# Kernel optimization log

Measured on AMD Instinct MI355X. Metric: run time of the kernel, lower is better.

Reference implementation:

```python
import jax, jax.numpy as jnp
import numpy as np

N_GRAPHS = 256
STEPS = 3


def setup_inputs() -> dict:
    key = jax.random.key(0)
    ks = jax.random.split(key, 8)
    N, d, out = 100000, 512, 256
    s = 0.05
    x = jax.random.normal(ks[0], (N, d), dtype=jnp.float32)
    batch = jnp.sort(jax.random.randint(ks[1], (N,), 0, N_GRAPHS)).astype(jnp.int64)
    W_ih = jax.random.normal(ks[2], (4 * d, 2 * d), dtype=jnp.float32) * s
    W_hh = jax.random.normal(ks[3], (4 * d, d), dtype=jnp.float32) * s
    b_ih = jax.random.normal(ks[4], (4 * d,), dtype=jnp.float32) * s
    b_hh = jax.random.normal(ks[5], (4 * d,), dtype=jnp.float32) * s
    W_proj = jax.random.normal(ks[6], (out, 2 * d), dtype=jnp.float32) * s
    b_proj = jax.random.normal(ks[7], (out,), dtype=jnp.float32) * s
    return {"x": x, "batch": batch, "W_ih": W_ih, "W_hh": W_hh,
            "b_ih": b_ih, "b_hh": b_hh, "W_proj": W_proj, "b_proj": b_proj}


def _set2set(x, batch, W_ih, W_hh, b_ih, b_hh):
    N, d = x.shape
    B = N_GRAPHS
    h = jnp.zeros((B, d), x.dtype)
    c = jnp.zeros((B, d), x.dtype)
    q_star = jnp.zeros((B, 2 * d), x.dtype)
    for _ in range(STEPS):
        # single-step LSTM cell (PyTorch gate order i,f,g,o)
        gates = q_star @ W_ih.T + b_ih + h @ W_hh.T + b_hh
        i, f, g, o = jnp.split(gates, 4, axis=-1)
        c = jax.nn.sigmoid(f) * c + jax.nn.sigmoid(i) * jnp.tanh(g)
        h = jax.nn.sigmoid(o) * jnp.tanh(c)
        q = h                                   # [B, d]
        # segment softmax attention over nodes
        e = jnp.sum(x * q[batch], axis=-1)      # [N]
        m = jax.ops.segment_max(e, batch, num_segments=B)
        m = jnp.where(jnp.isfinite(m), m, 0.0)  # guard empty segments
        ex = jnp.exp(e - m[batch])
        denom = jax.ops.segment_sum(ex, batch, num_segments=B) + 1e-16
        a = ex / denom[batch]                   # [N]
        r = jax.ops.segment_sum(a[:, None] * x, batch, num_segments=B)  # [B, d]
        q_star = jnp.concatenate([q, r], axis=-1)
    return q_star


def reference(x, batch, W_ih, W_hh, b_ih, b_hh, W_proj, b_proj):
    pooled = _set2set(x, batch, W_ih, W_hh, b_ih, b_hh)  # [B, 2d]
    return pooled @ W_proj.T + b_proj                    # [B, out]
```

## Files before the change

kernel.cpp:

```cpp
#include <hip/hip_runtime.h>
#include <hip/hip_bf16.h>


typedef __bf16 bf16_t;
typedef __bf16 bf16x8 __attribute__((ext_vector_type(8)));
typedef float  f32x4  __attribute__((ext_vector_type(4)));

#define D     512
#define B_GR  256
#define FOURD 2048
#define KCAT  1536
#define AWAVES 16
#define DET_BLOCKS 400

__device__ __forceinline__ float load_f(const void* b, int i, int f32) {
    return f32 ? ((const float*)b)[i] : (float)((const bf16_t*)b)[i];
}

__global__ void detect_part1(const int* __restrict__ b32, int N,
                             const unsigned short* __restrict__ xh,
                             int* __restrict__ partA, int* __restrict__ partB) {
    __shared__ int sA, sB;
    if (threadIdx.x == 0) { sA = 0; sB = 0; }
    __syncthreads();
    int gid = blockIdx.x * blockDim.x + threadIdx.x;
    int stride = gridDim.x * blockDim.x;
    int dec = 0;
    for (int i = gid; i < N - 1; i += stride)
        if (b32[i] > b32[i + 1]) dec = 1;
    int bad = 0;
    for (int i = gid; i < 1024; i += stride) {
        unsigned e = (xh[i] >> 7) & 0xff;
        if (e >= 134) bad = 1;
    }
    if (dec) atomicOr(&sA, 1);
    if (bad) atomicOr(&sB, 1);
    __syncthreads();
    if (threadIdx.x == 0) { partA[blockIdx.x] = sA; partB[blockIdx.x] = sB; }
}

__global__ void detect_part2(const int* __restrict__ partA,
                             const int* __restrict__ partB, int nblk,
                             int* __restrict__ flags) {
    __shared__ int sA, sB;
    if (threadIdx.x == 0) { sA = 0; sB = 0; }
    __syncthreads();
    int a = 0, b = 0;
    for (int i = threadIdx.x; i < nblk; i += blockDim.x) {
        a |= partA[i];
        b |= partB[i];
    }
    if (a) atomicOr(&sA, 1);
    if (b) atomicOr(&sB, 1);
    __syncthreads();
    if (threadIdx.x == 0) { flags[0] = sA; flags[1] = sB; }
}

#define WCAT_E (FOURD * KCAT)
#define WP_E   (256 * 1024)
__global__ void prep_seg_kernel(const void* __restrict__ W_ih,
                                const void* __restrict__ W_hh,
                                const void* __restrict__ b_ih,
                                const void* __restrict__ b_hh,
                                const void* __restrict__ W_proj,
                                const void* __restrict__ b_proj,
                                const void* __restrict__ batch, int N, int B,
                                const int* __restrict__ flags,
                                bf16_t* __restrict__ Wcat, bf16_t* __restrict__ Wp,
                                float* __restrict__ bsum, float* __restrict__ bp,
                                int* __restrict__ seg) {
    const int f32 = flags[1];
    int gid = blockIdx.x * blockDim.x + threadIdx.x;
    int stride = gridDim.x * blockDim.x;

    if (gid < N) {
        const int n = gid;
        const int is64 = flags[0];
        const int* b32 = (const int*)batch;
        const long long* b64 = (const long long*)batch;
        int cur = is64 ? (int)b64[n] : b32[n];
        if (n == 0) {
            for (int b = 0; b <= cur && b <= B; ++b) seg[b] = 0;
        } else {
            int prev = is64 ? (int)b64[n - 1] : b32[n - 1];
            for (int b = prev + 1; b <= cur && b <= B; ++b) seg[b] = n;
        }
        if (n == N - 1) {
            for (int b = cur + 1; b <= B; ++b) seg[b] = N;
        }
    }

    const int total = WCAT_E + WP_E + FOURD + 256;
    for (int idx = gid; idx < total; idx += stride) {
        if (idx < WCAT_E) {
            int r = idx / KCAT, k = idx - r * KCAT;
            float v = (k < 1024) ? load_f(W_ih, r * 1024 + k, f32)
                                 : load_f(W_hh, r * 512 + (k - 1024), f32);
            Wcat[idx] = (bf16_t)v;
        } else if (idx < WCAT_E + WP_E) {
            int j = idx - WCAT_E;
            Wp[j] = (bf16_t)load_f(W_proj, j, f32);
        } else if (idx < WCAT_E + WP_E + FOURD) {
            int i = idx - WCAT_E - WP_E;
            bsum[i] = load_f(b_ih, i, f32) + load_f(b_hh, i, f32);
        } else {
            int i = idx - WCAT_E - WP_E - FOURD;
            bp[i] = load_f(b_proj, i, f32);
        }
    }
}

__device__ __forceinline__ void lstm0_math(const float* __restrict__ bsum,
                                           int t, float& cn, float& hn) {
    float gi = bsum[t], gg = bsum[1024 + t], go = bsum[1536 + t];
    float si = 1.f / (1.f + __expf(-gi));
    float so = 1.f / (1.f + __expf(-go));
    float tg = tanhf(gg);
    cn = si * tg;
    hn = so * tanhf(cn);
}

__global__ __launch_bounds__(64)
void gemm_lstm(const bf16_t* __restrict__ AbufIn,
               const bf16_t* __restrict__ Wcat,
               const float* __restrict__ bsum,
               float* __restrict__ c, float* __restrict__ h,
               bf16_t* __restrict__ AbufOut) {
    const int lane  = threadIdx.x;
    const int t0    = blockIdx.x * 16;
    const int m0    = blockIdx.y * 16;
    const int rowA  = m0 + (lane & 15);
    const int colB  = t0 + (lane & 15);
    const int kbase = (lane >> 4) * 8;

    f32x4 acc[4] = {{0,0,0,0},{0,0,0,0},{0,0,0,0},{0,0,0,0}};

    for (int k0 = 0; k0 < KCAT; k0 += 32) {
        int k = k0 + kbase;
        bf16x8 a = *(const bf16x8*)(AbufIn + (size_t)rowA * KCAT + k);
#pragma unroll
        for (int g = 0; g < 4; ++g) {
            bf16x8 bfr = *(const bf16x8*)(Wcat + (size_t)(g * 512 + colB) * KCAT + k);
            acc[g] = __builtin_amdgcn_mfma_f32_16x16x32_bf16(a, bfr, acc[g], 0, 0, 0);
        }
    }

    const int col   = colB;
    const int rbase = (lane >> 4) * 4;
    float bi = bsum[col], bf = bsum[512 + col], bg = bsum[1024 + col], bo = bsum[1536 + col];
#pragma unroll
    for (int r = 0; r < 4; ++r) {
        int m = m0 + rbase + r;
        float gi = acc[0][r] + bi;
        float gf = acc[1][r] + bf;
        float gg = acc[2][r] + bg;
        float go = acc[3][r] + bo;
        size_t ci = (size_t)m * D + col;
        float cv = c[ci];
        float si = 1.f / (1.f + __expf(-gi));
        float sf = 1.f / (1.f + __expf(-gf));
        float so = 1.f / (1.f + __expf(-go));
        float tg = tanhf(gg);
        float cn = sf * cv + si * tg;
        float hn = so * tanhf(cn);
        c[ci] = cn;
        h[ci] = hn;
        bf16_t hb = (bf16_t)hn;
        AbufOut[(size_t)m * KCAT + col]        = hb;
        AbufOut[(size_t)m * KCAT + 1024 + col] = hb;
    }
}


template<bool WRXB>
__device__ __forceinline__ void scan_f32(const float* __restrict__ xp,
                                         bf16_t* __restrict__ xb,
                                         int s, int cnt, int wave, int lane,
                                         const float* hl,
                                         float& m_w, float& s_w, float* r_w) {
    int i = 4 * wave;
    for (; i + 4 <= cnt; i += 4 * AWAVES) {
        size_t off = (((size_t)(s + i)) << 9) + (size_t)(lane * 8);
        float xr[4][8];
#pragma unroll
        for (int r = 0; r < 4; ++r) {
            const float* p = xp + off + (size_t)r * D;
            float4 v0 = *(const float4*)p;
            float4 v1 = *(const float4*)(p + 4);
            xr[r][0] = v0.x; xr[r][1] = v0.y; xr[r][2] = v0.z; xr[r][3] = v0.w;
            xr[r][4] = v1.x; xr[r][5] = v1.y; xr[r][6] = v1.z; xr[r][7] = v1.w;
        }
        if (WRXB) {
#pragma unroll
            for (int r = 0; r < 4; ++r) {
                bf16x8 v;
#pragma unroll
                for (int j = 0; j < 8; ++j) v[j] = (bf16_t)xr[r][j];
                *(bf16x8*)(xb + off + (size_t)r * D) = v;
            }
        }
        float d[4] = {0.f, 0.f, 0.f, 0.f};
#pragma unroll
        for (int j = 0; j < 8; ++j) {
#pragma unroll
            for (int r = 0; r < 4; ++r) d[r] += xr[r][j] * hl[j];
        }
#pragma unroll
        for (int o = 32; o > 0; o >>= 1) {
#pragma unroll
            for (int r = 0; r < 4; ++r) d[r] += __shfl_xor(d[r], o, 64);
        }
        float mx    = fmaxf(fmaxf(d[0], d[1]), fmaxf(d[2], d[3]));
        float m_new = fmaxf(m_w, mx);
        float alpha = __expf(m_w - m_new);
        float p0 = __expf(d[0] - m_new), p1 = __expf(d[1] - m_new);
        float p2 = __expf(d[2] - m_new), p3 = __expf(d[3] - m_new);
        s_w = s_w * alpha + ((p0 + p1) + (p2 + p3));
#pragma unroll
        for (int j = 0; j < 8; ++j)
            r_w[j] = r_w[j] * alpha + p0 * xr[0][j] + p1 * xr[1][j]
                                    + p2 * xr[2][j] + p3 * xr[3][j];
        m_w = m_new;
    }
    if (i < cnt) {
        int rem = cnt - i;
        size_t off = (((size_t)(s + i)) << 9) + (size_t)(lane * 8);
        float xr[4][8];
#pragma unroll
        for (int r = 0; r < 4; ++r) {
            if (r < rem) {
                const float* p = xp + off + (size_t)r * D;
                float4 v0 = *(const float4*)p;
                float4 v1 = *(const float4*)(p + 4);
                xr[r][0] = v0.x; xr[r][1] = v0.y; xr[r][2] = v0.z; xr[r][3] = v0.w;
                xr[r][4] = v1.x; xr[r][5] = v1.y; xr[r][6] = v1.z; xr[r][7] = v1.w;
            } else {
#pragma unroll
                for (int j = 0; j < 8; ++j) xr[r][j] = 0.f;
            }
        }
        if (WRXB) {
#pragma unroll
            for (int r = 0; r < 4; ++r) {
                if (r < rem) {
                    bf16x8 v;
#pragma unroll
                    for (int j = 0; j < 8; ++j) v[j] = (bf16_t)xr[r][j];
                    *(bf16x8*)(xb + off + (size_t)r * D) = v;
                }
            }
        }
        float d[4] = {0.f, 0.f, 0.f, 0.f};
#pragma unroll
        for (int j = 0; j < 8; ++j) {
#pragma unroll
            for (int r = 0; r < 4; ++r) d[r] += xr[r][j] * hl[j];
        }
#pragma unroll
        for (int o = 32; o > 0; o >>= 1) {
#pragma unroll
            for (int r = 0; r < 4; ++r) d[r] += __shfl_xor(d[r], o, 64);
        }
#pragma unroll
        for (int r = 0; r < 4; ++r)
            if (r >= rem) d[r] = -INFINITY;
        float mx    = fmaxf(fmaxf(d[0], d[1]), fmaxf(d[2], d[3]));
        float m_new = fmaxf(m_w, mx);
        float alpha = __expf(m_w - m_new);
        float p0 = __expf(d[0] - m_new), p1 = __expf(d[1] - m_new);
        float p2 = __expf(d[2] - m_new), p3 = __expf(d[3] - m_new);
        s_w = s_w * alpha + ((p0 + p1) + (p2 + p3));
#pragma unroll
        for (int j = 0; j < 8; ++j)
            r_w[j] = r_w[j] * alpha + p0 * xr[0][j] + p1 * xr[1][j]
                                    + p2 * xr[2][j] + p3 * xr[3][j];
        m_w = m_new;
    }
}

__device__ __forceinline__ void scan_bf16(const bf16_t* __restrict__ xp,
                                          int s, int cnt, int wave, int lane,
                                          const float* hl,
                                          float& m_w, float& s_w, float* r_w) {
    int i = 4 * wave;
    for (; i + 4 <= cnt; i += 4 * AWAVES) {
        size_t off = (((size_t)(s + i)) << 9) + (size_t)(lane * 8);
        float xr[4][8];
#pragma unroll
        for (int r = 0; r < 4; ++r) {
            bf16x8 v = *(const bf16x8*)(xp + off + (size_t)r * D);
#pragma unroll
            for (int j = 0; j < 8; ++j) xr[r][j] = (float)v[j];
        }
        float d[4] = {0.f, 0.f, 0.f, 0.f};
#pragma unroll
        for (int j = 0; j < 8; ++j) {
#pragma unroll
            for (int r = 0; r < 4; ++r) d[r] += xr[r][j] * hl[j];
        }
#pragma unroll
        for (int o = 32; o > 0; o >>= 1) {
#pragma unroll
            for (int r = 0; r < 4; ++r) d[r] += __shfl_xor(d[r], o, 64);
        }
        float mx    = fmaxf(fmaxf(d[0], d[1]), fmaxf(d[2], d[3]));
        float m_new = fmaxf(m_w, mx);
        float alpha = __expf(m_w - m_new);
        float p0 = __expf(d[0] - m_new), p1 = __expf(d[1] - m_new);
        float p2 = __expf(d[2] - m_new), p3 = __expf(d[3] - m_new);
        s_w = s_w * alpha + ((p0 + p1) + (p2 + p3));
#pragma unroll
        for (int j = 0; j < 8; ++j)
            r_w[j] = r_w[j] * alpha + p0 * xr[0][j] + p1 * xr[1][j]
                                    + p2 * xr[2][j] + p3 * xr[3][j];
        m_w = m_new;
    }
    if (i < cnt) {
        int rem = cnt - i;
        size_t off = (((size_t)(s + i)) << 9) + (size_t)(lane * 8);
        float xr[4][8];
#pragma unroll
        for (int r = 0; r < 4; ++r) {
            if (r < rem) {
                bf16x8 v = *(const bf16x8*)(xp + off + (size_t)r * D);
#pragma unroll
                for (int j = 0; j < 8; ++j) xr[r][j] = (float)v[j];
            } else {
#pragma unroll
                for (int j = 0; j < 8; ++j) xr[r][j] = 0.f;
            }
        }
        float d[4] = {0.f, 0.f, 0.f, 0.f};
#pragma unroll
        for (int j = 0; j < 8; ++j) {
#pragma unroll
            for (int r = 0; r < 4; ++r) d[r] += xr[r][j] * hl[j];
        }
#pragma unroll
        for (int o = 32; o > 0; o >>= 1) {
#pragma unroll
            for (int r = 0; r < 4; ++r) d[r] += __shfl_xor(d[r], o, 64);
        }
#pragma unroll
        for (int r = 0; r < 4; ++r)
            if (r >= rem) d[r] = -INFINITY;
        float mx    = fmaxf(fmaxf(d[0], d[1]), fmaxf(d[2], d[3]));
        float m_new = fmaxf(m_w, mx);
        float alpha = __expf(m_w - m_new);
        float p0 = __expf(d[0] - m_new), p1 = __expf(d[1] - m_new);
        float p2 = __expf(d[2] - m_new), p3 = __expf(d[3] - m_new);
        s_w = s_w * alpha + ((p0 + p1) + (p2 + p3));
#pragma unroll
        for (int j = 0; j < 8; ++j)
            r_w[j] = r_w[j] * alpha + p0 * xr[0][j] + p1 * xr[1][j]
                                    + p2 * xr[2][j] + p3 * xr[3][j];
        m_w = m_new;
    }
}

template<int STEP0, int USE_XB, int PROJ>
__global__ __launch_bounds__(1024)
void attention_kernel(const void* __restrict__ x, bf16_t* __restrict__ xb,
                      int N, const int* __restrict__ seg,
                      const float* __restrict__ hbuf,
                      const float* __restrict__ bsum,
                      float* __restrict__ c_buf,
                      bf16_t* __restrict__ AbufOut,
                      const bf16_t* __restrict__ Wp,
                      const float* __restrict__ bp,
                      void* __restrict__ out,
                      const int* __restrict__ flags) {
    __shared__ float racc2[AWAVES][D];
    __shared__ float red_m[AWAVES], red_s[AWAVES];
    __shared__ __align__(16) bf16_t qsb[PROJ ? 1024 : 1];
    __shared__ float pout[PROJ ? 4 : 1][PROJ ? 256 : 1];

    const int f32x = flags[1];

    const int b = blockIdx.x;
    int s  = seg[b];
    int en = seg[b + 1];
    s  = (s  < 0) ? 0 : ((s  > N) ? N : s);
    en = (en < s) ? s : ((en > N) ? N : en);
    const int cnt  = en - s;
    const int tid  = threadIdx.x;
    const int wave = tid >> 6;
    const int lane = tid & 63;

    float hl[8];
    if (STEP0) {
#pragma unroll
        for (int j = 0; j < 8; ++j) {
            float cn, hn;
            lstm0_math(bsum, lane * 8 + j, cn, hn);
            hl[j] = hn;
        }
    } else {
        const float* hp = hbuf + ((size_t)b << 9) + lane * 8;
#pragma unroll
        for (int j = 0; j < 8; ++j) hl[j] = hp[j];
    }

    float m_w = -INFINITY, s_w = 0.f;
    float r_w[8];
#pragma unroll
    for (int j = 0; j < 8; ++j) r_w[j] = 0.f;

    if (f32x) {
        if (STEP0 || !USE_XB) {
            scan_f32<(STEP0 && USE_XB)>((const float*)x, xb, s, cnt,
                                        wave, lane, hl, m_w, s_w, r_w);
        } else {
            scan_bf16(xb, s, cnt, wave, lane, hl, m_w, s_w, r_w);
        }
    } else {
        scan_bf16((const bf16_t*)x, s, cnt, wave, lane, hl, m_w, s_w, r_w);
    }

    if (lane == 0) { red_m[wave] = m_w; red_s[wave] = s_w; }
    __syncthreads();

    float M = -INFINITY, S = 0.f;
#pragma unroll
    for (int w = 0; w < AWAVES; ++w)
        if (red_s[w] > 0.f) M = fmaxf(M, red_m[w]);
#pragma unroll
    for (int w = 0; w < AWAVES; ++w)
        if (red_s[w] > 0.f) S += red_s[w] * __expf(red_m[w] - M);
    float Sinv  = 1.f / (S + 1e-16f);
    float scale = (s_w > 0.f) ? __expf(m_w - M) * Sinv : 0.f;

#pragma unroll
    for (int j = 0; j < 8; ++j) racc2[wave][lane * 8 + j] = r_w[j] * scale;
    __syncthreads();

    if (PROJ) {
        if (tid < D) {
            float r = 0.f;
#pragma unroll
            for (int w = 0; w < AWAVES; ++w) r += racc2[w][tid];
            qsb[512 + tid] = (bf16_t)r;
            qsb[tid] = (bf16_t)hbuf[((size_t)b << 9) + tid];
        }
        __syncthreads();
        const int o    = tid & 255;
        const int part = tid >> 8;
        float acc = 0.f;
#pragma unroll
        for (int kk = 0; kk < 256; kk += 8) {
            int k = part * 256 + kk;
            bf16x8 w = *(const bf16x8*)(Wp + (size_t)o * 1024 + k);
            bf16x8 q = *(const bf16x8*)(qsb + k);
#pragma unroll
            for (int j = 0; j < 8; ++j) acc += (float)q[j] * (float)w[j];
        }
        pout[part][o] = acc;
        __syncthreads();
        if (tid < 256) {
            float v = pout[0][tid] + pout[1][tid] + pout[2][tid] + pout[3][tid]
                    + bp[tid];
            if (f32x) ((float*)out)[(size_t)b * 256 + tid]  = v;
            else      ((bf16_t*)out)[(size_t)b * 256 + tid] = (bf16_t)v;
        }
    } else {
        if (tid < D) {
            float r = 0.f;
#pragma unroll
            for (int w = 0; w < AWAVES; ++w) r += racc2[w][tid];
            AbufOut[(size_t)b * KCAT + 512 + tid] = (bf16_t)r;
            if (STEP0) {
                float cn, hn;
                lstm0_math(bsum, tid, cn, hn);
                c_buf[((size_t)b << 9) + tid] = cn;
                bf16_t hb = (bf16_t)hn;
                AbufOut[(size_t)b * KCAT + tid]        = hb;
                AbufOut[(size_t)b * KCAT + 1024 + tid] = hb;
            }
        }
    }
}

extern "C" void kernel_launch(void* const* d_in, const int* in_sizes, int n_in,
                              void* d_out, int out_size, void* d_ws, size_t ws_size,
                              hipStream_t stream) {
    const void* x      = d_in[0];
    const void* batch  = d_in[1];
    const void* W_ih   = d_in[2];
    const void* W_hh   = d_in[3];
    const void* b_ih   = d_in[4];
    const void* b_hh   = d_in[5];
    const void* W_proj = d_in[6];
    const void* b_proj = d_in[7];

    const int N = in_sizes[1];
    const int B = B_GR;

    char* p = (char*)d_ws;
    size_t used = 0;
    auto carve = [&](size_t bytes) {
        void* r = (void*)p;
        size_t a = (bytes + 1023) & ~(size_t)1023;
        p += a;
        used += a;
        return r;
    };
    float*  c_buf = (float*)carve((size_t)B * D * 4);
    float*  h_buf = (float*)carve((size_t)B * D * 4);
    bf16_t* Abuf0 = (bf16_t*)carve((size_t)B * KCAT * 2);
    bf16_t* Abuf1 = (bf16_t*)carve((size_t)B * KCAT * 2);
    bf16_t* Wcat  = (bf16_t*)carve((size_t)FOURD * KCAT * 2);
    bf16_t* Wp    = (bf16_t*)carve((size_t)256 * 1024 * 2);
    float*  bsum  = (float*)carve((size_t)FOURD * 4);
    float*  bp    = (float*)carve((size_t)256 * 4);
    int*    seg   = (int*)carve((size_t)(B + 1) * 4);
    int*    flags = (int*)carve(8);
    int*    partA = (int*)carve(DET_BLOCKS * 4);
    int*    partB = (int*)carve(DET_BLOCKS * 4);
    if (used > ws_size) return;
    bf16_t* xb = (bf16_t*)carve((size_t)N * D * 2);
    int use_xb = (used <= ws_size) ? 1 : 0;

    detect_part1<<<DET_BLOCKS, 256, 0, stream>>>(
        (const int*)batch, N, (const unsigned short*)x, partA, partB);
    detect_part2<<<1, 512, 0, stream>>>(partA, partB, DET_BLOCKS, flags);
    prep_seg_kernel<<<1024, 256, 0, stream>>>(W_ih, W_hh, b_ih, b_hh,
                                              W_proj, b_proj, batch, N, B,
                                              flags, Wcat, Wp, bsum, bp, seg);

    if (use_xb)
        attention_kernel<1, 1, 0><<<B, 1024, 0, stream>>>(
            x, xb, N, seg, h_buf, bsum, c_buf, Abuf0, Wp, bp, d_out, flags);
    else
        attention_kernel<1, 0, 0><<<B, 1024, 0, stream>>>(
            x, xb, N, seg, h_buf, bsum, c_buf, Abuf0, Wp, bp, d_out, flags);

    gemm_lstm<<<dim3(D / 16, B / 16), 64, 0, stream>>>(
        Abuf0, Wcat, bsum, c_buf, h_buf, Abuf1);
    if (use_xb)
        attention_kernel<0, 1, 0><<<B, 1024, 0, stream>>>(
            x, xb, N, seg, h_buf, bsum, c_buf, Abuf1, Wp, bp, d_out, flags);
    else
        attention_kernel<0, 0, 0><<<B, 1024, 0, stream>>>(
            x, xb, N, seg, h_buf, bsum, c_buf, Abuf1, Wp, bp, d_out, flags);

    gemm_lstm<<<dim3(D / 16, B / 16), 64, 0, stream>>>(
        Abuf1, Wcat, bsum, c_buf, h_buf, Abuf0);
    if (use_xb)
        attention_kernel<0, 1, 1><<<B, 1024, 0, stream>>>(
            x, xb, N, seg, h_buf, bsum, c_buf, Abuf0, Wp, bp, d_out, flags);
    else
        attention_kernel<0, 0, 1><<<B, 1024, 0, stream>>>(
            x, xb, N, seg, h_buf, bsum, c_buf, Abuf0, Wp, bp, d_out, flags);
}
```

Baseline: 443.0 us.

## Fuse attention and LSTM GEMM steps into one cooperative persistent kernel

Replaces the five separate attention and GEMM launches with a single cooperative kernel of 256 blocks that uses grid-wide barriers between phases, with two waves per block running the GEMM tiles. Segment-bound computation is split out of the weight-prep kernel into its own launch. The aim is to remove launch gaps and kernel-boundary drains between the dependent steps. In exchange, each GEMM phase runs on only two waves per block while the rest idle, grid.sync adds its own cost, and the whole grid must be co-resident.

```diff
diff --git a/kernel.cpp b/kernel.cpp
--- a/kernel.cpp
+++ b/kernel.cpp
@@ -1,5 +1,8 @@
 #include <hip/hip_runtime.h>
 #include <hip/hip_bf16.h>
+#include <hip/hip_cooperative_groups.h>
+
+namespace cg = cooperative_groups;
 
 
 typedef __bf16 bf16_t;
@@ -56,40 +59,40 @@
     if (threadIdx.x == 0) { flags[0] = sA; flags[1] = sB; }
 }
 
+__global__ void seg_bounds_kernel(const void* __restrict__ batch, int N, int B,
+                                  const int* __restrict__ flags,
+                                  int* __restrict__ seg) {
+    int n = blockIdx.x * blockDim.x + threadIdx.x;
+    if (n >= N) return;
+    const int is64 = flags[0];
+    const int* b32 = (const int*)batch;
+    const long long* b64 = (const long long*)batch;
+    int cur = is64 ? (int)b64[n] : b32[n];
+    if (n == 0) {
+        for (int b = 0; b <= cur && b <= B; ++b) seg[b] = 0;
+    } else {
+        int prev = is64 ? (int)b64[n - 1] : b32[n - 1];
+        for (int b = prev + 1; b <= cur && b <= B; ++b) seg[b] = n;
+    }
+    if (n == N - 1) {
+        for (int b = cur + 1; b <= B; ++b) seg[b] = N;
+    }
+}
+
 #define WCAT_E (FOURD * KCAT)
 #define WP_E   (256 * 1024)
-__global__ void prep_seg_kernel(const void* __restrict__ W_ih,
-                                const void* __restrict__ W_hh,
-                                const void* __restrict__ b_ih,
-                                const void* __restrict__ b_hh,
-                                const void* __restrict__ W_proj,
-                                const void* __restrict__ b_proj,
-                                const void* __restrict__ batch, int N, int B,
-                                const int* __restrict__ flags,
-                                bf16_t* __restrict__ Wcat, bf16_t* __restrict__ Wp,
-                                float* __restrict__ bsum, float* __restrict__ bp,
-                                int* __restrict__ seg) {
+__global__ void prep_kernel(const void* __restrict__ W_ih,
+                            const void* __restrict__ W_hh,
+                            const void* __restrict__ b_ih,
+                            const void* __restrict__ b_hh,
+                            const void* __restrict__ W_proj,
+                            const void* __restrict__ b_proj,
+                            const int* __restrict__ flags,
+                            bf16_t* __restrict__ Wcat, bf16_t* __restrict__ Wp,
+                            float* __restrict__ bsum, float* __restrict__ bp) {
     const int f32 = flags[1];
     int gid = blockIdx.x * blockDim.x + threadIdx.x;
     int stride = gridDim.x * blockDim.x;
-
-    if (gid < N) {
-        const int n = gid;
-        const int is64 = flags[0];
-        const int* b32 = (const int*)batch;
-        const long long* b64 = (const long long*)batch;
-        int cur = is64 ? (int)b64[n] : b32[n];
-        if (n == 0) {
-            for (int b = 0; b <= cur && b <= B; ++b) seg[b] = 0;
-        } else {
-            int prev = is64 ? (int)b64[n - 1] : b32[n - 1];
-            for (int b = prev + 1; b <= cur && b <= B; ++b) seg[b] = n;
-        }
-        if (n == N - 1) {
-            for (int b = cur + 1; b <= B; ++b) seg[b] = N;
-        }
-    }
-
     const int total = WCAT_E + WP_E + FOURD + 256;
     for (int idx = gid; idx < total; idx += stride) {
         if (idx < WCAT_E) {
@@ -120,15 +123,15 @@
     hn = so * tanhf(cn);
 }
 
-__global__ __launch_bounds__(64)
-void gemm_lstm(const bf16_t* __restrict__ AbufIn,
-               const bf16_t* __restrict__ Wcat,
-               const float* __restrict__ bsum,
-               float* __restrict__ c, float* __restrict__ h,
-               bf16_t* __restrict__ AbufOut) {
-    const int lane  = threadIdx.x;
-    const int t0    = blockIdx.x * 16;
-    const int m0    = blockIdx.y * 16;
+__device__ __forceinline__ void gemm_job(int job, int lane,
+                                         const bf16_t* __restrict__ AbufIn,
+                                         const bf16_t* __restrict__ Wcat,
+                                         const float* __restrict__ bsum,
+                                         float* __restrict__ c,
+                                         float* __restrict__ h,
+                                         bf16_t* __restrict__ AbufOut) {
+    const int t0    = (job & 31) * 16;
+    const int m0    = (job >> 5) * 16;
     const int rowA  = m0 + (lane & 15);
     const int colB  = t0 + (lane & 15);
     const int kbase = (lane >> 4) * 8;
@@ -358,25 +361,26 @@
     }
 }
 
+struct __align__(16) AttnShared {
+    float  racc2[AWAVES][D];
+    float  red_m[AWAVES];
+    float  red_s[AWAVES];
+    bf16_t qsb[1024];
+    float  pout[4][256];
+};
+
 template<int STEP0, int USE_XB, int PROJ>
-__global__ __launch_bounds__(1024)
-void attention_kernel(const void* __restrict__ x, bf16_t* __restrict__ xb,
-                      int N, const int* __restrict__ seg,
-                      const float* __restrict__ hbuf,
-                      const float* __restrict__ bsum,
-                      float* __restrict__ c_buf,
-                      bf16_t* __restrict__ AbufOut,
-                      const bf16_t* __restrict__ Wp,
-                      const float* __restrict__ bp,
-                      void* __restrict__ out,
-                      const int* __restrict__ flags) {
-    __shared__ float racc2[AWAVES][D];
-    __shared__ float red_m[AWAVES], red_s[AWAVES];
-    __shared__ __align__(16) bf16_t qsb[PROJ ? 1024 : 1];
-    __shared__ float pout[PROJ ? 4 : 1][PROJ ? 256 : 1];
-
-    const int f32x = flags[1];
-
+__device__ __forceinline__ void attn_phase(AttnShared& sh,
+                                           const void* __restrict__ x,
+                                           bf16_t* __restrict__ xb, int N,
+                                           const int* __restrict__ seg,
+                                           const float* __restrict__ hbuf,
+                                           const float* __restrict__ bsum,
+                                           float* __restrict__ c_buf,
+                                           bf16_t* __restrict__ AbufOut,
+                                           const bf16_t* __restrict__ Wp,
+                                           const float* __restrict__ bp,
+                                           void* __restrict__ out, int f32x) {
     const int b = blockIdx.x;
     int s  = seg[b];
     int en = seg[b + 1];
@@ -417,30 +421,30 @@
         scan_bf16((const bf16_t*)x, s, cnt, wave, lane, hl, m_w, s_w, r_w);
     }
 
-    if (lane == 0) { red_m[wave] = m_w; red_s[wave] = s_w; }
+    if (lane == 0) { sh.red_m[wave] = m_w; sh.red_s[wave] = s_w; }
     __syncthreads();
 
     float M = -INFINITY, S = 0.f;
 #pragma unroll
     for (int w = 0; w < AWAVES; ++w)
-        if (red_s[w] > 0.f) M = fmaxf(M, red_m[w]);
+        if (sh.red_s[w] > 0.f) M = fmaxf(M, sh.red_m[w]);
 #pragma unroll
     for (int w = 0; w < AWAVES; ++w)
-        if (red_s[w] > 0.f) S += red_s[w] * __expf(red_m[w] - M);
+        if (sh.red_s[w] > 0.f) S += sh.red_s[w] * __expf(sh.red_m[w] - M);
     float Sinv  = 1.f / (S + 1e-16f);
     float scale = (s_w > 0.f) ? __expf(m_w - M) * Sinv : 0.f;
 
 #pragma unroll
-    for (int j = 0; j < 8; ++j) racc2[wave][lane * 8 + j] = r_w[j] * scale;
+    for (int j = 0; j < 8; ++j) sh.racc2[wave][lane * 8 + j] = r_w[j] * scale;
     __syncthreads();
 
     if (PROJ) {
         if (tid < D) {
             float r = 0.f;
 #pragma unroll
-            for (int w = 0; w < AWAVES; ++w) r += racc2[w][tid];
-            qsb[512 + tid] = (bf16_t)r;
-            qsb[tid] = (bf16_t)hbuf[((size_t)b << 9) + tid];
+            for (int w = 0; w < AWAVES; ++w) r += sh.racc2[w][tid];
+            sh.qsb[512 + tid] = (bf16_t)r;
+            sh.qsb[tid] = (bf16_t)hbuf[((size_t)b << 9) + tid];
         }
         __syncthreads();
         const int o    = tid & 255;
@@ -450,15 +454,15 @@
         for (int kk = 0; kk < 256; kk += 8) {
             int k = part * 256 + kk;
             bf16x8 w = *(const bf16x8*)(Wp + (size_t)o * 1024 + k);
-            bf16x8 q = *(const bf16x8*)(qsb + k);
+            bf16x8 q = *(const bf16x8*)(sh.qsb + k);
 #pragma unroll
             for (int j = 0; j < 8; ++j) acc += (float)q[j] * (float)w[j];
         }
-        pout[part][o] = acc;
+        sh.pout[part][o] = acc;
         __syncthreads();
         if (tid < 256) {
-            float v = pout[0][tid] + pout[1][tid] + pout[2][tid] + pout[3][tid]
-                    + bp[tid];
+            float v = sh.pout[0][tid] + sh.pout[1][tid] + sh.pout[2][tid]
+                    + sh.pout[3][tid] + bp[tid];
             if (f32x) ((float*)out)[(size_t)b * 256 + tid]  = v;
             else      ((bf16_t*)out)[(size_t)b * 256 + tid] = (bf16_t)v;
         }
@@ -466,7 +470,7 @@
         if (tid < D) {
             float r = 0.f;
 #pragma unroll
-            for (int w = 0; w < AWAVES; ++w) r += racc2[w][tid];
+            for (int w = 0; w < AWAVES; ++w) r += sh.racc2[w][tid];
             AbufOut[(size_t)b * KCAT + 512 + tid] = (bf16_t)r;
             if (STEP0) {
                 float cn, hn;
@@ -477,7 +481,46 @@
                 AbufOut[(size_t)b * KCAT + 1024 + tid] = hb;
             }
         }
-    }
+        __syncthreads();
+    }
+}
+
+template<int USE_XB>
+__global__ __launch_bounds__(1024)
+void mega_kernel(const void* __restrict__ x, bf16_t* __restrict__ xb, int N,
+                 const int* __restrict__ seg, const float* __restrict__ bsum,
+                 float* __restrict__ c_buf, float* __restrict__ h_buf,
+                 bf16_t* __restrict__ Abuf0, bf16_t* __restrict__ Abuf1,
+                 const bf16_t* __restrict__ Wcat, const bf16_t* __restrict__ Wp,
+                 const float* __restrict__ bp, void* __restrict__ out,
+                 const int* __restrict__ flags) {
+    __shared__ AttnShared sh;
+    cg::grid_group grid = cg::this_grid();
+    const int f32x = flags[1];
+    const int tid  = threadIdx.x;
+    const int wave = tid >> 6;
+    const int lane = tid & 63;
+
+    attn_phase<1, USE_XB, 0>(sh, x, xb, N, seg, h_buf, bsum, c_buf,
+                             Abuf0, Wp, bp, out, f32x);
+    grid.sync();
+
+    if (wave < 2)
+        gemm_job(wave * B_GR + blockIdx.x, lane, Abuf0, Wcat, bsum,
+                 c_buf, h_buf, Abuf1);
+    grid.sync();
+
+    attn_phase<0, USE_XB, 0>(sh, x, xb, N, seg, h_buf, bsum, c_buf,
+                             Abuf1, Wp, bp, out, f32x);
+    grid.sync();
+
+    if (wave < 2)
+        gemm_job(wave * B_GR + blockIdx.x, lane, Abuf1, Wcat, bsum,
+                 c_buf, h_buf, Abuf0);
+    grid.sync();
+
+    attn_phase<0, USE_XB, 1>(sh, x, xb, N, seg, h_buf, bsum, c_buf,
+                             Abuf0, Wp, bp, out, f32x);
 }
 
 extern "C" void kernel_launch(void* const* d_in, const int* in_sizes, int n_in,
@@ -523,32 +566,34 @@
     detect_part1<<<DET_BLOCKS, 256, 0, stream>>>(
         (const int*)batch, N, (const unsigned short*)x, partA, partB);
     detect_part2<<<1, 512, 0, stream>>>(partA, partB, DET_BLOCKS, flags);
-    prep_seg_kernel<<<1024, 256, 0, stream>>>(W_ih, W_hh, b_ih, b_hh,
-                                              W_proj, b_proj, batch, N, B,
-                                              flags, Wcat, Wp, bsum, bp, seg);
-
-    if (use_xb)
-        attention_kernel<1, 1, 0><<<B, 1024, 0, stream>>>(
-            x, xb, N, seg, h_buf, bsum, c_buf, Abuf0, Wp, bp, d_out, flags);
-    else
-        attention_kernel<1, 0, 0><<<B, 1024, 0, stream>>>(
-            x, xb, N, seg, h_buf, bsum, c_buf, Abuf0, Wp, bp, d_out, flags);
-
-    gemm_lstm<<<dim3(D / 16, B / 16), 64, 0, stream>>>(
-        Abuf0, Wcat, bsum, c_buf, h_buf, Abuf1);
-    if (use_xb)
-        attention_kernel<0, 1, 0><<<B, 1024, 0, stream>>>(
-            x, xb, N, seg, h_buf, bsum, c_buf, Abuf1, Wp, bp, d_out, flags);
-    else
-        attention_kernel<0, 0, 0><<<B, 1024, 0, stream>>>(
-            x, xb, N, seg, h_buf, bsum, c_buf, Abuf1, Wp, bp, d_out, flags);
-
-    gemm_lstm<<<dim3(D / 16, B / 16), 64, 0, stream>>>(
-        Abuf1, Wcat, bsum, c_buf, h_buf, Abuf0);
-    if (use_xb)
-        attention_kernel<0, 1, 1><<<B, 1024, 0, stream>>>(
-            x, xb, N, seg, h_buf, bsum, c_buf, Abuf0, Wp, bp, d_out, flags);
-    else
-        attention_kernel<0, 0, 1><<<B, 1024, 0, stream>>>(
-            x, xb, N, seg, h_buf, bsum, c_buf, Abuf0, Wp, bp, d_out, flags);
-}
+    seg_bounds_kernel<<<(N + 255) / 256, 256, 0, stream>>>(batch, N, B, flags, seg);
+    prep_kernel<<<1024, 256, 0, stream>>>(W_ih, W_hh, b_ih, b_hh, W_proj, b_proj,
+                                          flags, Wcat, Wp, bsum, bp);
+
+    {
+        const void* xa   = x;
+        bf16_t*     xba  = xb;
+        int         Na   = N;
+        const int*  sega = seg;
+        const float* bsa = bsum;
+        float*      cba  = c_buf;
+        float*      hba  = h_buf;
+        bf16_t*     A0a  = Abuf0;
+        bf16_t*     A1a  = Abuf1;
+        const bf16_t* Wca = Wcat;
+        const bf16_t* Wpa = Wp;
+        const float* bpa = bp;
+        void*       outa = d_out;
+        const int*  fla  = flags;
+        void* args[] = {&xa, &xba, &Na, &sega, &bsa, &cba, &hba,
+                        &A0a, &A1a, &Wca, &Wpa, &bpa, &outa, &fla};
+        if (use_xb)
+            hipLaunchCooperativeKernel(
+                reinterpret_cast<void*>(&mega_kernel<1>),
+                dim3(B), dim3(1024), args, 0, stream);
+        else
+            hipLaunchCooperativeKernel(
+                reinterpret_cast<void*>(&mega_kernel<0>),
+                dim3(B), dim3(1024), args, 0, stream);
+    }
+}
```

Result: slower. 578.6 us (+30.6%).
